# Kernel tuning notes

Hardware: AMD Instinct MI355X
Metric: run time of the kernel (lower is better)

## Reference

```python
import jax, jax.numpy as jnp
import numpy as np

D_MODEL = 768
N_HEADS = 12
HEAD = 64
B, T = 2, 2048


def setup_inputs() -> dict:
    key = jax.random.key(0)
    k1, k2, k3 = jax.random.split(key, 3)
    x = jax.random.normal(k1, (B, T, D_MODEL), dtype=jnp.float32)
    W1 = jax.random.normal(k2, (3 * D_MODEL, D_MODEL), dtype=jnp.float32) * (1.0 / np.sqrt(D_MODEL))
    b1 = jnp.zeros((3 * D_MODEL,), dtype=jnp.float32)
    W2 = jax.random.normal(k3, (D_MODEL, D_MODEL), dtype=jnp.float32) * (1.0 / np.sqrt(D_MODEL))
    b2 = jnp.zeros((D_MODEL,), dtype=jnp.float32)
    return {"x": x, "W1": W1, "b1": b1, "W2": W2, "b2": b2}


def reference(x, W1, b1, W2, b2):
    Bx, Tx, C = x.shape
    qkv = jnp.einsum('btc,fc->btf', x, W1) + b1            # (B,T,3C)
    q, k, v = jnp.split(qkv, 3, axis=-1)
    # (B,T,H,Dh) -> (B,H,T,Dh)
    q = q.reshape(Bx, Tx, N_HEADS, HEAD).transpose(0, 2, 1, 3)
    k = k.reshape(Bx, Tx, N_HEADS, HEAD).transpose(0, 2, 1, 3)
    v = v.reshape(Bx, Tx, N_HEADS, HEAD).transpose(0, 2, 1, 3)
    scale = 1.0 / np.sqrt(HEAD)
    scores = jnp.einsum('bhqd,bhkd->bhqk', q, k) * scale   # (B,H,T,T)
    causal = jnp.tril(jnp.ones((Tx, Tx), dtype=bool))
    scores = jnp.where(causal, scores, jnp.finfo(scores.dtype).min)
    attn = jax.nn.softmax(scores, axis=-1)
    o = jnp.einsum('bhqk,bhkd->bhqd', attn, v)             # (B,H,T,Dh)
    o = o.transpose(0, 2, 1, 3).reshape(Bx, Tx, C)
    return jnp.einsum('btc,fc->btf', o, W2) + b2
```

## Files before the change

### kernel.cpp

```cpp
#include <hip/hip_runtime.h>


typedef float f32x4 __attribute__((ext_vector_type(4)));
typedef __bf16 bf16x8 __attribute__((ext_vector_type(8)));

#define D_MODEL 768
#define F3 2304
#define NHEADS 12
#define HEAD 64
#define BB 2
#define TT 2048
#define MROWS (BB*TT)
#define KDIM 768
#define LOG2E 1.44269504f
#define NX (MROWS*D_MODEL)
#define NW1 (F3*KDIM)
#define NW2 (D_MODEL*KDIM)
#define NHT 16
#define NOF (BB*NHEADS*NHT*64*64)
#define NLF (BB*NHEADS*NHT*64)
#define NZF (NOF+NLF)

__device__ __forceinline__ unsigned short f2bf(float f) {
    unsigned int u = __float_as_uint(f);
    u += 0x7fffu + ((u >> 16) & 1u);
    return (unsigned short)(u >> 16);
}
__device__ __forceinline__ unsigned int pack2bf(float a, float b) {
    unsigned int ua = __float_as_uint(a), ub = __float_as_uint(b);
    ua += 0x7fffu + ((ua >> 16) & 1u);
    ub += 0x7fffu + ((ub >> 16) & 1u);
    return (ua >> 16) | (ub & 0xffff0000u);
}

__device__ __forceinline__ void async_copy16(unsigned short* lds, const unsigned short* g) {
    __builtin_amdgcn_global_load_lds(
        (const __attribute__((address_space(1))) unsigned int*)(const void*)g,
        (__attribute__((address_space(3))) unsigned int*)(void*)lds,
        16, 0, 0);
}

__global__ void prep(const float* __restrict__ x, const float* __restrict__ W1,
                     const float* __restrict__ W2, unsigned short* __restrict__ xb,
                     unsigned short* __restrict__ w1b, unsigned short* __restrict__ w2b,
                     float* __restrict__ zf) {
    const int i4 = (blockIdx.x * blockDim.x + threadIdx.x) * 4;
    const float* src; unsigned short* dst; int off;
    if (i4 < NX)                  { src = x;  dst = xb;  off = i4; }
    else if (i4 < NX + NW1)       { src = W1; dst = w1b; off = i4 - NX; }
    else if (i4 < NX + NW1 + NW2) { src = W2; dst = w2b; off = i4 - NX - NW1; }
    else if (i4 < NX + NW1 + NW2 + NZF) {
        f32x4 z = {};
        *(f32x4*)(zf + (i4 - (NX + NW1 + NW2))) = z;
        return;
    }
    else return;
    float4 v = *(const float4*)(src + off);
    uint2 o;
    o.x = pack2bf(v.x, v.y);
    o.y = pack2bf(v.z, v.w);
    *(uint2*)(dst + off) = o;
}

__global__ __launch_bounds__(256, 4) void gemm1(
    const unsigned short* __restrict__ A, const unsigned short* __restrict__ Bw,
    const float* __restrict__ bias, int K,
    unsigned short* __restrict__ Qb, unsigned short* __restrict__ Kb,
    unsigned short* __restrict__ VT)
{
    __shared__ unsigned short As[128*64];
    __shared__ unsigned short Bs[128*64];
    const int tid  = threadIdx.x;
    const int wave = tid >> 6;
    const int lane = tid & 63;
    const int quad = lane >> 4;
    const int l16  = lane & 15;
    const int m0 = blockIdx.x * 128;
    const int n0 = blockIdx.y * 128;
    const int wm = (wave >> 1) * 64;
    const int wn = (wave & 1) * 64;

    f32x4 acc[4][4] = {};

    const unsigned short* Ablk = A + (size_t)m0 * K;
    const unsigned short* Bblk = Bw + (size_t)n0 * K;
    const int srow = (lane >> 3);
    const int scol = ((lane & 7) ^ srow) * 8;

    for (int k0 = 0; k0 < K; k0 += 64) {
        #pragma unroll
        for (int q2 = 0; q2 < 4; ++q2) {
            int t = wave * 4 + q2;
            int row = t * 8 + srow;
            async_copy16(As + t * 512, Ablk + (size_t)row * K + k0 + scol);
            async_copy16(Bs + t * 512, Bblk + (size_t)row * K + k0 + scol);
        }
        asm volatile("s_waitcnt vmcnt(0)" ::: "memory");
        __syncthreads();

        #pragma unroll
        for (int kc2 = 0; kc2 < 2; ++kc2) {
            const int pos = ((kc2*4 + quad) ^ (l16 & 7)) * 8;
            bf16x8 a[4], b[4];
            #pragma unroll
            for (int i = 0; i < 4; ++i)
                a[i] = *(const bf16x8*)(As + (wm + i*16 + l16)*64 + pos);
            #pragma unroll
            for (int j = 0; j < 4; ++j)
                b[j] = *(const bf16x8*)(Bs + (wn + j*16 + l16)*64 + pos);
            #pragma unroll
            for (int i = 0; i < 4; ++i)
                #pragma unroll
                for (int j = 0; j < 4; ++j)
                    acc[i][j] = __builtin_amdgcn_mfma_f32_16x16x32_bf16(a[i], b[j], acc[i][j], 0, 0, 0);
        }
        __syncthreads();
    }

    const int seg = blockIdx.y / 6;
    if (seg < 2) {
        #pragma unroll
        for (int j = 0; j < 4; ++j) {
            const int n = n0 + wn + j*16 + l16;
            const float bv = bias[n];
            const int f = n - seg * 768;
            const int h = f >> 6, d = f & 63;
            #pragma unroll
            for (int i = 0; i < 4; ++i)
                #pragma unroll
                for (int r = 0; r < 4; ++r) {
                    const int m = m0 + wm + i*16 + quad*4 + r;
                    const int b = m >> 11, t = m & 2047;
                    const size_t idx = (((size_t)(b*NHEADS + h)) * TT + t) * HEAD + d;
                    const float v = acc[i][j][r] + bv;
                    if (seg == 0) Qb[idx] = f2bf(v * (0.125f * LOG2E));
                    else          Kb[idx] = f2bf(v);
                }
        }
    } else {
        #pragma unroll
        for (int j = 0; j < 4; ++j) {
            const int n = n0 + wn + j*16 + l16;
            const float bv = bias[n];
            const int f = n - 1536;
            const int h = f >> 6, d = f & 63;
            #pragma unroll
            for (int i = 0; i < 4; ++i) {
                const int m = m0 + wm + i*16 + quad*4;
                const int b = m >> 11, t = m & 2047;
                uint2 pk;
                pk.x = pack2bf(acc[i][j][0] + bv, acc[i][j][1] + bv);
                pk.y = pack2bf(acc[i][j][2] + bv, acc[i][j][3] + bv);
                *(uint2*)(VT + ((size_t)(b*NHEADS + h) * HEAD + d) * TT + t) = pk;
            }
        }
    }
}

__global__ __launch_bounds__(256, 4) void gemm2(
    const unsigned short* __restrict__ A, const unsigned short* __restrict__ Bw,
    const float* __restrict__ bias, int K, float* __restrict__ Cout)
{
    __shared__ unsigned short As[64*64];
    __shared__ unsigned short Bs[128*64];
    const int tid  = threadIdx.x;
    const int wave = tid >> 6;
    const int lane = tid & 63;
    const int quad = lane >> 4;
    const int l16  = lane & 15;
    const int m0 = blockIdx.x * 64;
    const int n0 = blockIdx.y * 128;
    const int wm = (wave >> 1) * 32;
    const int wn = (wave & 1) * 64;

    f32x4 acc[2][4] = {};

    const unsigned short* Ablk = A + (size_t)m0 * K;
    const unsigned short* Bblk = Bw + (size_t)n0 * K;
    const int srow = tid >> 3;
    const int scol = ((tid & 7) ^ (srow & 7)) * 8;

    for (int k0 = 0; k0 < K; k0 += 64) {
        #pragma unroll
        for (int i = 0; i < 2; ++i)
            async_copy16(As + i*2048 + tid*8,
                         Ablk + (size_t)(i*32 + srow) * K + k0 + scol);
        #pragma unroll
        for (int i = 0; i < 4; ++i)
            async_copy16(Bs + i*2048 + tid*8,
                         Bblk + (size_t)(i*32 + srow) * K + k0 + scol);
        asm volatile("s_waitcnt vmcnt(0)" ::: "memory");
        __syncthreads();

        #pragma unroll
        for (int kc2 = 0; kc2 < 2; ++kc2) {
            const int pos = ((kc2*4 + quad) ^ (l16 & 7)) * 8;
            bf16x8 a[2], b[4];
            #pragma unroll
            for (int i = 0; i < 2; ++i)
                a[i] = *(const bf16x8*)(As + (wm + i*16 + l16)*64 + pos);
            #pragma unroll
            for (int j = 0; j < 4; ++j)
                b[j] = *(const bf16x8*)(Bs + (wn + j*16 + l16)*64 + pos);
            #pragma unroll
            for (int i = 0; i < 2; ++i)
                #pragma unroll
                for (int j = 0; j < 4; ++j)
                    acc[i][j] = __builtin_amdgcn_mfma_f32_16x16x32_bf16(a[i], b[j], acc[i][j], 0, 0, 0);
        }
        __syncthreads();
    }

    #pragma unroll
    for (int j = 0; j < 4; ++j) {
        const int n = n0 + wn + j*16 + l16;
        const float bv = bias[n];
        #pragma unroll
        for (int i = 0; i < 2; ++i)
            #pragma unroll
            for (int r = 0; r < 4; ++r) {
                const int m = m0 + wm + i*16 + quad*4 + r;
                Cout[(size_t)m * D_MODEL + n] = acc[i][j][r] + bv;
            }
    }
}

__global__ __launch_bounds__(256, 2) void attn(
    const unsigned short* __restrict__ Qb, const unsigned short* __restrict__ Kb,
    const unsigned short* __restrict__ VT, unsigned short* __restrict__ Ob,
    float* __restrict__ Of, float* __restrict__ Lf)
{
    __shared__ unsigned short Ks[128*64];
    __shared__ unsigned short Vt[64*128];
    __shared__ unsigned short Ps[4][16*128];

    const int tid  = threadIdx.x;
    const int wave = tid >> 6;
    const int lane = tid & 63;
    const int quad = lane >> 4;
    const int l16  = lane & 15;
    const int j    = blockIdx.x;
    const int bh   = blockIdx.y;
    const int i    = j & 15;
    const bool isA = (j < 16);
    const int half = i >> 1;
    const int split = 8 - half;
    const size_t hbase = (size_t)bh * TT * HEAD;

    const int krow = tid >> 3;
    const int kchunk = ((tid & 7) ^ (krow & 7)) * 8;
    const int vrow = tid >> 4;
    const int vchunk = ((tid & 15) ^ vrow) * 8;

    const int nseg = isA ? 2 : 1;
    for (int segi = 0; segi < nseg; ++segi) {
        int qt, kb, ke; bool full;
        if (isA) {
            if (segi == 0) { qt = i;      kb = 0;     ke = half + 1;  full = true;  }
            else           { qt = 31 - i; kb = 0;     ke = split;     full = false; }
        } else             { qt = 31 - i; kb = split; ke = 16 - half; full = false; }
        const bool domask = (ke == (qt >> 1) + 1);
        const int qg = qt*64 + wave*16 + l16;

        bf16x8 qreg[2];
        {
            const unsigned short* qp = Qb + hbase + (size_t)qg * HEAD + quad*8;
            qreg[0] = *(const bf16x8*)(qp);
            qreg[1] = *(const bf16x8*)(qp + 32);
        }

        f32x4 oacc[4] = {};
        float lst = 0.f;

        for (int kt = kb; kt < ke; ++kt) {
            __syncthreads();

            const unsigned short* ksrc = Kb + hbase + (size_t)kt * 128 * HEAD;
            #pragma unroll
            for (int ii = 0; ii < 4; ++ii)
                async_copy16(Ks + ii*2048 + tid*8,
                             ksrc + (size_t)(ii*32 + krow) * 64 + kchunk);
            #pragma unroll
            for (int ii = 0; ii < 4; ++ii)
                async_copy16(Vt + ii*2048 + tid*8,
                             VT + hbase + (size_t)(ii*16 + vrow) * TT + kt*128 + vchunk);
            asm volatile("s_waitcnt vmcnt(0)" ::: "memory");
            __syncthreads();

            f32x4 s[8] = {};
            #pragma unroll
            for (int kc2 = 0; kc2 < 2; ++kc2) {
                bf16x8 bq = qreg[kc2];
                const int pos = ((kc2*4 + quad) ^ (l16 & 7)) * 8;
                #pragma unroll
                for (int nt = 0; nt < 8; ++nt) {
                    bf16x8 ak = *(const bf16x8*)(Ks + (nt*16 + l16)*64 + pos);
                    s[nt] = __builtin_amdgcn_mfma_f32_16x16x32_bf16(ak, bq, s[nt], 0, 0, 0);
                }
            }

            if (domask && kt == ke - 1) {
                const int kq = kt*128 + quad*4;
                #pragma unroll
                for (int nt = 0; nt < 8; ++nt)
                    #pragma unroll
                    for (int r = 0; r < 4; ++r)
                        if (kq + nt*16 + r > qg) s[nt][r] = -1e30f;
            }

            float rsum = 0.f;
            uint2 pck[8];
            #pragma unroll
            for (int nt = 0; nt < 8; ++nt) {
                const float p0 = exp2f(s[nt][0]);
                const float p1 = exp2f(s[nt][1]);
                const float p2 = exp2f(s[nt][2]);
                const float p3 = exp2f(s[nt][3]);
                rsum += (p0 + p1) + (p2 + p3);
                pck[nt].x = (__float_as_uint(p0) >> 16) | (__float_as_uint(p1) & 0xffff0000u);
                pck[nt].y = (__float_as_uint(p2) >> 16) | (__float_as_uint(p3) & 0xffff0000u);
            }
            rsum += __shfl_xor(rsum, 16);
            rsum += __shfl_xor(rsum, 32);
            lst += rsum;

            #pragma unroll
            for (int nt = 0; nt < 8; ++nt)
                *(uint2*)(&Ps[wave][l16*128 + ((nt*2 + (quad>>1)) ^ l16)*8 + (quad&1)*4]) = pck[nt];

            #pragma unroll
            for (int kc = 0; kc < 4; ++kc) {
                bf16x8 ap = *(const bf16x8*)(&Ps[wave][l16*128 + ((kc*4 + quad) ^ l16)*8]);
                const int vp = ((kc*4 + quad) ^ l16) * 8;
                #pragma unroll
                for (int dt = 0; dt < 4; ++dt) {
                    bf16x8 bv = *(const bf16x8*)(Vt + (dt*16 + l16)*128 + vp);
                    oacc[dt] = __builtin_amdgcn_mfma_f32_16x16x32_bf16(ap, bv, oacc[dt], 0, 0, 0);
                }
            }
        }

        if (full) {
            const float linv = 1.0f / lst;
            float lr[4];
            #pragma unroll
            for (int r = 0; r < 4; ++r) lr[r] = __shfl(linv, quad*4 + r);
            const int b = bh / NHEADS, h = bh % NHEADS;
            #pragma unroll
            for (int r = 0; r < 4; ++r) {
                const int m = b * TT + qt*64 + wave*16 + quad*4 + r;
                #pragma unroll
                for (int dt = 0; dt < 4; ++dt)
                    Ob[(size_t)m * D_MODEL + h*HEAD + dt*16 + l16] = f2bf(oacc[dt][r] * lr[r]);
            }
        } else {
            const int qtl = qt - 16;
            float* op = Of + (((size_t)(bh*NHT + qtl))*64 + wave*16)*64;
            #pragma unroll
            for (int dt = 0; dt < 4; ++dt)
                #pragma unroll
                for (int r = 0; r < 4; ++r)
                    atomicAdd(&op[(quad*4 + r)*64 + dt*16 + l16], oacc[dt][r]);
            if (quad == 0)
                atomicAdd(&Lf[((size_t)(bh*NHT + qtl))*64 + wave*16 + l16], lst);
        }
    }
}

__global__ __launch_bounds__(256) void fixup(
    const float* __restrict__ Of, const float* __restrict__ Lf,
    unsigned short* __restrict__ Ob)
{
    const int qtl = blockIdx.x;
    const int bh  = blockIdx.y;
    const int t   = threadIdx.x;
    const int r   = t >> 2;
    const int c0  = (t & 3) * 16;
    const float linv = 1.0f / Lf[((size_t)(bh*NHT + qtl))*64 + r];
    const float* src = Of + (((size_t)(bh*NHT + qtl))*64 + r)*64 + c0;
    const int b = bh / NHEADS, h = bh % NHEADS;
    const int m = b*TT + (16 + qtl)*64 + r;
    unsigned short* dst = Ob + (size_t)m * D_MODEL + h*HEAD + c0;
    f32x4 v0 = *(const f32x4*)(src);
    f32x4 v1 = *(const f32x4*)(src + 4);
    f32x4 v2 = *(const f32x4*)(src + 8);
    f32x4 v3 = *(const f32x4*)(src + 12);
    uint4 o0, o1;
    o0.x = pack2bf(v0[0]*linv, v0[1]*linv);
    o0.y = pack2bf(v0[2]*linv, v0[3]*linv);
    o0.z = pack2bf(v1[0]*linv, v1[1]*linv);
    o0.w = pack2bf(v1[2]*linv, v1[3]*linv);
    o1.x = pack2bf(v2[0]*linv, v2[1]*linv);
    o1.y = pack2bf(v2[2]*linv, v2[3]*linv);
    o1.z = pack2bf(v3[0]*linv, v3[1]*linv);
    o1.w = pack2bf(v3[2]*linv, v3[3]*linv);
    *(uint4*)(dst)     = o0;
    *(uint4*)(dst + 8) = o1;
}

extern "C" void kernel_launch(void* const* d_in, const int* in_sizes, int n_in,
                              void* d_out, int out_size, void* d_ws, size_t ws_size,
                              hipStream_t stream) {
    const float* x  = (const float*)d_in[0];
    const float* W1 = (const float*)d_in[1];
    const float* b1 = (const float*)d_in[2];
    const float* W2 = (const float*)d_in[3];
    const float* b2 = (const float*)d_in[4];
    float* out = (float*)d_out;

    unsigned short* ws = (unsigned short*)d_ws;
    unsigned short* xb  = ws;
    unsigned short* w1b = xb  + (size_t)NX;
    unsigned short* w2b = w1b + (size_t)NW1;
    unsigned short* Qb  = w2b + (size_t)NW2;
    unsigned short* Kb  = Qb + (size_t)BB*NHEADS*TT*HEAD;
    unsigned short* VT  = Kb + (size_t)BB*NHEADS*TT*HEAD;
    unsigned short* Ob  = VT + (size_t)BB*NHEADS*TT*HEAD;
    float* Of = (float*)(Ob + (size_t)NX);
    float* Lf = Of + (size_t)NOF;

    prep<<<((NX + NW1 + NW2 + NZF)/4 + 255)/256, 256, 0, stream>>>(
        x, W1, W2, xb, w1b, w2b, Of);

    gemm1<<<dim3(MROWS/128, F3/128), 256, 0, stream>>>(
        xb, w1b, b1, KDIM, Qb, Kb, VT);

    attn<<<dim3(32, BB*NHEADS), 256, 0, stream>>>(Qb, Kb, VT, Ob, Of, Lf);

    fixup<<<dim3(NHT, BB*NHEADS), 256, 0, stream>>>(Of, Lf, Ob);

    gemm2<<<dim3(MROWS/64, D_MODEL/128), 256, 0, stream>>>(
        Ob, w2b, b2, KDIM, out);
}
```

Before: 152.1 us.

## Replace atomic split-K partials with separate buffers and keep P in registers

The attention kernel now writes its two partial outputs (A and B halves of the split query tiles) into separate buffers with plain stores instead of atomics into a zeroed buffer. Fixup sums the two buffers, so prep no longer has to zero the accumulators. P is fed straight from registers into the MFMA with a matching V permutation, which removes the LDS round trip and the Ps shared buffer. Block indices are remapped so each XCD handles contiguous heads, and launch bounds are raised to 4 for occupancy. In exchange there is more workspace and fixup memory traffic, and V is now read with split 8-byte loads.

```diff
diff --git a/kernel.cpp b/kernel.cpp
--- a/kernel.cpp
+++ b/kernel.cpp
@@ -3,6 +3,7 @@
 
 typedef float f32x4 __attribute__((ext_vector_type(4)));
 typedef __bf16 bf16x8 __attribute__((ext_vector_type(8)));
+typedef unsigned int u32x4 __attribute__((ext_vector_type(4)));
 
 #define D_MODEL 768
 #define F3 2304
@@ -19,7 +20,6 @@
 #define NHT 16
 #define NOF (BB*NHEADS*NHT*64*64)
 #define NLF (BB*NHEADS*NHT*64)
-#define NZF (NOF+NLF)
 
 __device__ __forceinline__ unsigned short f2bf(float f) {
     unsigned int u = __float_as_uint(f);
@@ -42,18 +42,12 @@
 
 __global__ void prep(const float* __restrict__ x, const float* __restrict__ W1,
                      const float* __restrict__ W2, unsigned short* __restrict__ xb,
-                     unsigned short* __restrict__ w1b, unsigned short* __restrict__ w2b,
-                     float* __restrict__ zf) {
+                     unsigned short* __restrict__ w1b, unsigned short* __restrict__ w2b) {
     const int i4 = (blockIdx.x * blockDim.x + threadIdx.x) * 4;
     const float* src; unsigned short* dst; int off;
     if (i4 < NX)                  { src = x;  dst = xb;  off = i4; }
     else if (i4 < NX + NW1)       { src = W1; dst = w1b; off = i4 - NX; }
     else if (i4 < NX + NW1 + NW2) { src = W2; dst = w2b; off = i4 - NX - NW1; }
-    else if (i4 < NX + NW1 + NW2 + NZF) {
-        f32x4 z = {};
-        *(f32x4*)(zf + (i4 - (NX + NW1 + NW2))) = z;
-        return;
-    }
     else return;
     float4 v = *(const float4*)(src + off);
     uint2 o;
@@ -225,22 +219,27 @@
     }
 }
 
-__global__ __launch_bounds__(256, 2) void attn(
+__global__ __launch_bounds__(256, 4) void attn(
     const unsigned short* __restrict__ Qb, const unsigned short* __restrict__ Kb,
     const unsigned short* __restrict__ VT, unsigned short* __restrict__ Ob,
-    float* __restrict__ Of, float* __restrict__ Lf)
+    float* __restrict__ OfA, float* __restrict__ OfB,
+    float* __restrict__ LfA, float* __restrict__ LfB)
 {
     __shared__ unsigned short Ks[128*64];
     __shared__ unsigned short Vt[64*128];
-    __shared__ unsigned short Ps[4][16*128];
 
     const int tid  = threadIdx.x;
     const int wave = tid >> 6;
     const int lane = tid & 63;
     const int quad = lane >> 4;
     const int l16  = lane & 15;
-    const int j    = blockIdx.x;
-    const int bh   = blockIdx.y;
+
+    const int F    = blockIdx.y * 32 + blockIdx.x;
+    const int xcd  = F & 7;
+    const int slot = F >> 3;
+    const int bh   = xcd * 3 + (slot >> 5);
+    const int j    = slot & 31;
+
     const int i    = j & 15;
     const bool isA = (j < 16);
     const int half = i >> 1;
@@ -325,16 +324,19 @@
             lst += rsum;
 
             #pragma unroll
-            for (int nt = 0; nt < 8; ++nt)
-                *(uint2*)(&Ps[wave][l16*128 + ((nt*2 + (quad>>1)) ^ l16)*8 + (quad&1)*4]) = pck[nt];
-
-            #pragma unroll
             for (int kc = 0; kc < 4; ++kc) {
-                bf16x8 ap = *(const bf16x8*)(&Ps[wave][l16*128 + ((kc*4 + quad) ^ l16)*8]);
-                const int vp = ((kc*4 + quad) ^ l16) * 8;
+                u32x4 pw = {pck[2*kc].x, pck[2*kc].y, pck[2*kc+1].x, pck[2*kc+1].y};
+                bf16x8 ap = __builtin_bit_cast(bf16x8, pw);
+                const int g1 = 4*kc + (quad >> 1);
+                const int c1 = ((g1     ^ l16) * 8) + (quad & 1) * 4;
+                const int c2 = (((g1+2) ^ l16) * 8) + (quad & 1) * 4;
                 #pragma unroll
                 for (int dt = 0; dt < 4; ++dt) {
-                    bf16x8 bv = *(const bf16x8*)(Vt + (dt*16 + l16)*128 + vp);
+                    const unsigned short* vr = Vt + (dt*16 + l16)*128;
+                    uint2 lo = *(const uint2*)(vr + c1);
+                    uint2 hi = *(const uint2*)(vr + c2);
+                    u32x4 vv = {lo.x, lo.y, hi.x, hi.y};
+                    bf16x8 bv = __builtin_bit_cast(bf16x8, vv);
                     oacc[dt] = __builtin_amdgcn_mfma_f32_16x16x32_bf16(ap, bv, oacc[dt], 0, 0, 0);
                 }
             }
@@ -355,20 +357,22 @@
             }
         } else {
             const int qtl = qt - 16;
-            float* op = Of + (((size_t)(bh*NHT + qtl))*64 + wave*16)*64;
+            float* op = (isA ? OfA : OfB)
+                        + (((size_t)(bh*NHT + qtl))*64 + wave*16)*64;
             #pragma unroll
             for (int dt = 0; dt < 4; ++dt)
                 #pragma unroll
                 for (int r = 0; r < 4; ++r)
-                    atomicAdd(&op[(quad*4 + r)*64 + dt*16 + l16], oacc[dt][r]);
+                    op[(quad*4 + r)*64 + dt*16 + l16] = oacc[dt][r];
             if (quad == 0)
-                atomicAdd(&Lf[((size_t)(bh*NHT + qtl))*64 + wave*16 + l16], lst);
+                (isA ? LfA : LfB)[((size_t)(bh*NHT + qtl))*64 + wave*16 + l16] = lst;
         }
     }
 }
 
 __global__ __launch_bounds__(256) void fixup(
-    const float* __restrict__ Of, const float* __restrict__ Lf,
+    const float* __restrict__ OfA, const float* __restrict__ OfB,
+    const float* __restrict__ LfA, const float* __restrict__ LfB,
     unsigned short* __restrict__ Ob)
 {
     const int qtl = blockIdx.x;
@@ -376,24 +380,33 @@
     const int t   = threadIdx.x;
     const int r   = t >> 2;
     const int c0  = (t & 3) * 16;
-    const float linv = 1.0f / Lf[((size_t)(bh*NHT + qtl))*64 + r];
-    const float* src = Of + (((size_t)(bh*NHT + qtl))*64 + r)*64 + c0;
+    const size_t lidx = ((size_t)(bh*NHT + qtl))*64 + r;
+    const float linv = 1.0f / (LfA[lidx] + LfB[lidx]);
+    const size_t base = (((size_t)(bh*NHT + qtl))*64 + r)*64 + c0;
+    const float* sa = OfA + base;
+    const float* sb = OfB + base;
     const int b = bh / NHEADS, h = bh % NHEADS;
     const int m = b*TT + (16 + qtl)*64 + r;
     unsigned short* dst = Ob + (size_t)m * D_MODEL + h*HEAD + c0;
-    f32x4 v0 = *(const f32x4*)(src);
-    f32x4 v1 = *(const f32x4*)(src + 4);
-    f32x4 v2 = *(const f32x4*)(src + 8);
-    f32x4 v3 = *(const f32x4*)(src + 12);
     uint4 o0, o1;
-    o0.x = pack2bf(v0[0]*linv, v0[1]*linv);
-    o0.y = pack2bf(v0[2]*linv, v0[3]*linv);
-    o0.z = pack2bf(v1[0]*linv, v1[1]*linv);
-    o0.w = pack2bf(v1[2]*linv, v1[3]*linv);
-    o1.x = pack2bf(v2[0]*linv, v2[1]*linv);
-    o1.y = pack2bf(v2[2]*linv, v2[3]*linv);
-    o1.z = pack2bf(v3[0]*linv, v3[1]*linv);
-    o1.w = pack2bf(v3[2]*linv, v3[3]*linv);
+    {
+        f32x4 a0 = *(const f32x4*)(sa);      f32x4 b0 = *(const f32x4*)(sb);
+        f32x4 a1 = *(const f32x4*)(sa + 4);  f32x4 b1 = *(const f32x4*)(sb + 4);
+        f32x4 v0 = a0 + b0, v1 = a1 + b1;
+        o0.x = pack2bf(v0[0]*linv, v0[1]*linv);
+        o0.y = pack2bf(v0[2]*linv, v0[3]*linv);
+        o0.z = pack2bf(v1[0]*linv, v1[1]*linv);
+        o0.w = pack2bf(v1[2]*linv, v1[3]*linv);
+    }
+    {
+        f32x4 a2 = *(const f32x4*)(sa + 8);  f32x4 b2 = *(const f32x4*)(sb + 8);
+        f32x4 a3 = *(const f32x4*)(sa + 12); f32x4 b3 = *(const f32x4*)(sb + 12);
+        f32x4 v2 = a2 + b2, v3 = a3 + b3;
+        o1.x = pack2bf(v2[0]*linv, v2[1]*linv);
+        o1.y = pack2bf(v2[2]*linv, v2[3]*linv);
+        o1.z = pack2bf(v3[0]*linv, v3[1]*linv);
+        o1.w = pack2bf(v3[2]*linv, v3[3]*linv);
+    }
     *(uint4*)(dst)     = o0;
     *(uint4*)(dst + 8) = o1;
 }
@@ -416,18 +429,21 @@
     unsigned short* Kb  = Qb + (size_t)BB*NHEADS*TT*HEAD;
     unsigned short* VT  = Kb + (size_t)BB*NHEADS*TT*HEAD;
     unsigned short* Ob  = VT + (size_t)BB*NHEADS*TT*HEAD;
-    float* Of = (float*)(Ob + (size_t)NX);
-    float* Lf = Of + (size_t)NOF;
-
-    prep<<<((NX + NW1 + NW2 + NZF)/4 + 255)/256, 256, 0, stream>>>(
-        x, W1, W2, xb, w1b, w2b, Of);
+    float* OfA = (float*)(Ob + (size_t)NX);
+    float* OfB = OfA + (size_t)NOF;
+    float* LfA = OfB + (size_t)NOF;
+    float* LfB = LfA + (size_t)NLF;
+
+    prep<<<((NX + NW1 + NW2)/4 + 255)/256, 256, 0, stream>>>(
+        x, W1, W2, xb, w1b, w2b);
 
     gemm1<<<dim3(MROWS/128, F3/128), 256, 0, stream>>>(
         xb, w1b, b1, KDIM, Qb, Kb, VT);
 
-    attn<<<dim3(32, BB*NHEADS), 256, 0, stream>>>(Qb, Kb, VT, Ob, Of, Lf);
-
-    fixup<<<dim3(NHT, BB*NHEADS), 256, 0, stream>>>(Of, Lf, Ob);
+    attn<<<dim3(32, BB*NHEADS), 256, 0, stream>>>(
+        Qb, Kb, VT, Ob, OfA, OfB, LfA, LfB);
+
+    fixup<<<dim3(NHT, BB*NHEADS), 256, 0, stream>>>(OfA, OfB, LfA, LfB, Ob);
 
     gemm2<<<dim3(MROWS/64, D_MODEL/128), 256, 0, stream>>>(
         Ob, w2b, b2, KDIM, out);
```

Result: no change. 149.5 us (-1.7%).
